# Performance work log

Hardware: AMD Instinct MI355X
Metric: run time of the kernel (lower is better)

The kernel has to match this reference:

```python
import jax, jax.numpy as jnp
import numpy as np

T = 100  # number of time steps
B = 256
F = 4096

def setup_inputs() -> dict:
    key = jax.random.key(0)
    k1, k2 = jax.random.split(key)
    x = jax.random.uniform(k1, (B, F), dtype=jnp.float32)
    delays = jax.random.uniform(k2, (F,), dtype=jnp.float32)
    return {"x": x, "delays": delays}

def reference(x, delays):
    # spike_times: [B, F] int, truncation toward zero like torch .long()
    st = ((1.0 - x * delays[None, :]) * (T - 1)).astype(jnp.int32)
    st = jnp.clip(st, 0, T - 1)
    # one-hot over time axis -> [B, T, F]
    t_axis = jnp.arange(T, dtype=jnp.int32)[None, :, None]  # [1, T, 1]
    spikes = (t_axis == st[:, None, :]).astype(jnp.float32)
    return spikes
```

## Files before the change

### kernel.cpp

```cpp
#include <hip/hip_runtime.h>

constexpr int T = 100;
constexpr int B = 256;
constexpr int F = 4096;
constexpr int F4 = F / 4;

typedef float floatx4 __attribute__((ext_vector_type(4)));

__global__ __launch_bounds__(256) void spike_kernel(
    const float* __restrict__ x,
    const float* __restrict__ delays,
    float* __restrict__ out)
{
    const int idx = blockIdx.x * blockDim.x + threadIdx.x;
    const int f4  = idx & (F4 - 1);
    const int b   = idx >> 10;

    const floatx4 xv = reinterpret_cast<const floatx4*>(x)[idx];
    const floatx4 dv = reinterpret_cast<const floatx4*>(delays)[f4];

    auto spike_time = [](float xi, float di) -> int {
        float p  = __fmul_rn(xi, di);
        float s  = __fsub_rn(1.0f, p);
        float v  = __fmul_rn(s, 99.0f);
        int   st = (int)v;
        st = st < 0 ? 0 : st;
        st = st > (T - 1) ? (T - 1) : st;
        return st;
    };

    const int st0 = spike_time(xv.x, dv.x);
    const int st1 = spike_time(xv.y, dv.y);
    const int st2 = spike_time(xv.z, dv.z);
    const int st3 = spike_time(xv.w, dv.w);

    floatx4* outp = reinterpret_cast<floatx4*>(out) + (size_t)b * T * F4 + f4;

#pragma unroll 4
    for (int t = 0; t < T; ++t) {
        floatx4 v;
        v.x = (t == st0) ? 1.0f : 0.0f;
        v.y = (t == st1) ? 1.0f : 0.0f;
        v.z = (t == st2) ? 1.0f : 0.0f;
        v.w = (t == st3) ? 1.0f : 0.0f;
        outp[(size_t)t * F4] = v;
    }
}

extern "C" void kernel_launch(void* const* d_in, const int* in_sizes, int n_in,
                              void* d_out, int out_size, void* d_ws, size_t ws_size,
                              hipStream_t stream)
{
    const float* x      = reinterpret_cast<const float*>(d_in[0]);
    const float* delays = reinterpret_cast<const float*>(d_in[1]);
    float* out          = reinterpret_cast<float*>(d_out);

    const int n_threads = B * F4;
    const int block = 256;
    const int grid  = n_threads / block;
    spike_kernel<<<grid, block, 0, stream>>>(x, delays, out);
}
```

Measured before the change: 408.5 us.

## Remap blocks to write full contiguous rows over time chunks

```diff
diff --git a/kernel.cpp b/kernel.cpp
--- a/kernel.cpp
+++ b/kernel.cpp
@@ -1,23 +1,25 @@
 #include <hip/hip_runtime.h>
 
-constexpr int T = 100;
-constexpr int B = 256;
-constexpr int F = 4096;
+constexpr int T  = 100;
+constexpr int B  = 256;
+constexpr int F  = 4096;
 constexpr int F4 = F / 4;
 
 typedef float floatx4 __attribute__((ext_vector_type(4)));
 
-__global__ __launch_bounds__(256) void spike_kernel(
+constexpr int BLOCK     = 256;
+constexpr int TCHUNK    = 25;
+constexpr int BLK_PER_B = T / TCHUNK;
+constexpr int NBLK      = B * BLK_PER_B;
+
+__global__ __launch_bounds__(BLOCK) void spike_kernel(
     const float* __restrict__ x,
     const float* __restrict__ delays,
     float* __restrict__ out)
 {
-    const int idx = blockIdx.x * blockDim.x + threadIdx.x;
-    const int f4  = idx & (F4 - 1);
-    const int b   = idx >> 10;
-
-    const floatx4 xv = reinterpret_cast<const floatx4*>(x)[idx];
-    const floatx4 dv = reinterpret_cast<const floatx4*>(delays)[f4];
+    const int tid = threadIdx.x;
+    const int b   = blockIdx.x >> 2;
+    const int t0  = (blockIdx.x & 3) * TCHUNK;
 
     auto spike_time = [](float xi, float di) -> int {
         float p  = __fmul_rn(xi, di);
@@ -29,21 +31,31 @@
         return st;
     };
 
-    const int st0 = spike_time(xv.x, dv.x);
-    const int st1 = spike_time(xv.y, dv.y);
-    const int st2 = spike_time(xv.z, dv.z);
-    const int st3 = spike_time(xv.w, dv.w);
+    int st[4][4];
+#pragma unroll
+    for (int j = 0; j < 4; ++j) {
+        const int f4s = (j << 8) + tid;
+        const floatx4 xv = reinterpret_cast<const floatx4*>(x)[(b << 10) + f4s];
+        const floatx4 dv = reinterpret_cast<const floatx4*>(delays)[f4s];
+        st[j][0] = spike_time(xv.x, dv.x);
+        st[j][1] = spike_time(xv.y, dv.y);
+        st[j][2] = spike_time(xv.z, dv.z);
+        st[j][3] = spike_time(xv.w, dv.w);
+    }
 
-    floatx4* outp = reinterpret_cast<floatx4*>(out) + (size_t)b * T * F4 + f4;
+    floatx4* outp = reinterpret_cast<floatx4*>(out)
+                  + (((size_t)(b * T + t0)) << 10) + tid;
 
-#pragma unroll 4
-    for (int t = 0; t < T; ++t) {
-        floatx4 v;
-        v.x = (t == st0) ? 1.0f : 0.0f;
-        v.y = (t == st1) ? 1.0f : 0.0f;
-        v.z = (t == st2) ? 1.0f : 0.0f;
-        v.w = (t == st3) ? 1.0f : 0.0f;
-        outp[(size_t)t * F4] = v;
+    for (int t = t0; t < t0 + TCHUNK; ++t, outp += F4) {
+#pragma unroll
+        for (int j = 0; j < 4; ++j) {
+            floatx4 v;
+            v.x = (t == st[j][0]) ? 1.0f : 0.0f;
+            v.y = (t == st[j][1]) ? 1.0f : 0.0f;
+            v.z = (t == st[j][2]) ? 1.0f : 0.0f;
+            v.w = (t == st[j][3]) ? 1.0f : 0.0f;
+            outp[j << 8] = v;
+        }
     }
 }
 
@@ -55,8 +67,5 @@
     const float* delays = reinterpret_cast<const float*>(d_in[1]);
     float* out          = reinterpret_cast<float*>(d_out);
 
-    const int n_threads = B * F4;
-    const int block = 256;
-    const int grid  = n_threads / block;
-    spike_kernel<<<grid, block, 0, stream>>>(x, delays, out);
+    spike_kernel<<<NBLK, BLOCK, 0, stream>>>(x, delays, out);
 }
```

New measurement: 418.6 us. +2.5%, slower.

## Split into packed spike-time precompute and grid-stride contiguous output writer

Applied to the files above, without the earlier changes.

```diff
diff --git a/kernel.cpp b/kernel.cpp
--- a/kernel.cpp
+++ b/kernel.cpp
@@ -1,13 +1,74 @@
 #include <hip/hip_runtime.h>
 
-constexpr int T = 100;
-constexpr int B = 256;
-constexpr int F = 4096;
+constexpr int T  = 100;
+constexpr int B  = 256;
+constexpr int F  = 4096;
 constexpr int F4 = F / 4;
 
-typedef float floatx4 __attribute__((ext_vector_type(4)));
+typedef float        floatx4 __attribute__((ext_vector_type(4)));
+typedef unsigned int u32;
 
-__global__ __launch_bounds__(256) void spike_kernel(
+__global__ __launch_bounds__(256) void build_st(
+    const float* __restrict__ x,
+    const float* __restrict__ delays,
+    u32* __restrict__ stw)
+{
+    const int idx = blockIdx.x * 256 + threadIdx.x;
+    const int f4  = idx & (F4 - 1);
+
+    const floatx4 xv = reinterpret_cast<const floatx4*>(x)[idx];
+    const floatx4 dv = reinterpret_cast<const floatx4*>(delays)[f4];
+
+    auto sti = [](float xi, float di) -> u32 {
+        float p  = __fmul_rn(xi, di);
+        float s  = __fsub_rn(1.0f, p);
+        float v  = __fmul_rn(s, 99.0f);
+        int   st = (int)v;
+        st = st < 0 ? 0 : st;
+        st = st > (T - 1) ? (T - 1) : st;
+        return (u32)st;
+    };
+
+    const u32 w = sti(xv.x, dv.x)
+                | (sti(xv.y, dv.y) << 8)
+                | (sti(xv.z, dv.z) << 16)
+                | (sti(xv.w, dv.w) << 24);
+    stw[idx] = w;
+}
+
+constexpr int BLOCK  = 256;
+constexpr int NBLK   = 2048;
+constexpr int G      = NBLK * BLOCK;
+constexpr int TOTAL4 = B * T * F4;
+constexpr int NITER  = TOTAL4 / G;
+
+__global__ __launch_bounds__(BLOCK) void write_spikes(
+    const u32* __restrict__ stw,
+    float* __restrict__ out)
+{
+    const int tid0 = blockIdx.x * BLOCK + threadIdx.x;
+    const int f4   = tid0 & (F4 - 1);
+    floatx4* out4  = reinterpret_cast<floatx4*>(out);
+
+    int idx = tid0;
+    for (int k = 0; k < NITER; ++k, idx += G) {
+        const int bt = idx >> 10;
+        const int b  = (bt * 5243) >> 19;
+        const int t  = bt - b * 100;
+
+        const u32 w = stw[(b << 10) | f4];
+
+        floatx4 v;
+        v.x = (t == (int)( w        & 255u)) ? 1.0f : 0.0f;
+        v.y = (t == (int)((w >> 8)  & 255u)) ? 1.0f : 0.0f;
+        v.z = (t == (int)((w >> 16) & 255u)) ? 1.0f : 0.0f;
+        v.w = (t == (int)( w >> 24        )) ? 1.0f : 0.0f;
+
+        out4[idx] = v;
+    }
+}
+
+__global__ __launch_bounds__(256) void spike_kernel_fb(
     const float* __restrict__ x,
     const float* __restrict__ delays,
     float* __restrict__ out)
@@ -28,14 +89,12 @@
         st = st > (T - 1) ? (T - 1) : st;
         return st;
     };
-
     const int st0 = spike_time(xv.x, dv.x);
     const int st1 = spike_time(xv.y, dv.y);
     const int st2 = spike_time(xv.z, dv.z);
     const int st3 = spike_time(xv.w, dv.w);
 
     floatx4* outp = reinterpret_cast<floatx4*>(out) + (size_t)b * T * F4 + f4;
-
 #pragma unroll 4
     for (int t = 0; t < T; ++t) {
         floatx4 v;
@@ -55,8 +114,12 @@
     const float* delays = reinterpret_cast<const float*>(d_in[1]);
     float* out          = reinterpret_cast<float*>(d_out);
 
-    const int n_threads = B * F4;
-    const int block = 256;
-    const int grid  = n_threads / block;
-    spike_kernel<<<grid, block, 0, stream>>>(x, delays, out);
+    const size_t needed = (size_t)B * F4 * sizeof(u32);
+    if (ws_size >= needed && d_ws != nullptr) {
+        u32* stw = reinterpret_cast<u32*>(d_ws);
+        build_st<<<B * F4 / 256, 256, 0, stream>>>(x, delays, stw);
+        write_spikes<<<NBLK, BLOCK, 0, stream>>>(stw, out);
+    } else {
+        spike_kernel_fb<<<B * F4 / 256, 256, 0, stream>>>(x, delays, out);
+    }
 }
```

New measurement: 403.5 us. Within noise of the previous version (-1.2%).
